# Optimization experiments

Hardware: AMD Instinct MI355X
Metric: run time of the kernel (lower is better)

Reference implementation:

```python
import jax, jax.numpy as jnp
import numpy as np

SIZE = 768
SMALL = SIZE // 4 + 1  # 193
N_ROWS = 16 * 512      # 8192 flattened timesteps
N_CODES = 30000
N_PAIRS = 300000


def setup_inputs() -> dict:
    key = jax.random.key(0)
    ks = jax.random.split(key, 10)
    rnn_output = jax.random.normal(ks[0], (16, 512, SIZE), dtype=jnp.float32)
    weight = jax.random.normal(ks[1], (N_CODES, SIZE + 1), dtype=jnp.float32) * 0.02
    weight1 = jax.random.normal(ks[2], (N_CODES, SMALL), dtype=jnp.float32) * 0.02
    idx0 = jnp.stack([
        jax.random.randint(ks[3], (N_PAIRS,), 0, N_ROWS),
        jax.random.randint(ks[4], (N_PAIRS,), 0, N_CODES),
    ], axis=1).astype(jnp.int64)
    y0 = (jax.random.uniform(ks[5], (N_PAIRS,)) < 0.5).astype(jnp.float32)
    idx1 = jnp.stack([
        jax.random.randint(ks[6], (N_PAIRS,), 0, N_ROWS),
        jax.random.randint(ks[7], (N_PAIRS,), 0, N_CODES),
    ], axis=1).astype(jnp.int64)
    y1 = (jax.random.uniform(ks[8], (N_PAIRS,)) < 0.5).astype(jnp.float32)
    seen0 = jnp.zeros((N_PAIRS,), dtype=jnp.float32)
    seen1 = jnp.zeros((N_PAIRS,), dtype=jnp.float32)
    return {"rnn_output": rnn_output, "weight": weight, "weight1": weight1,
            "idx0": idx0, "y0": y0, "seen0": seen0,
            "idx1": idx1, "y1": y1, "seen1": seen1}


def _embedding_dot(features, table, idx):
    # gather feature rows and code-embedding rows, then row-wise dot -> [N]
    f = features[idx[:, 0]]   # [N, D]
    w = table[idx[:, 1]]      # [N, D]
    return jnp.sum(f * w, axis=-1)


def _bce_logits_sum(logits, targets):
    # stable: log(1 + exp(x)) - x*y, summed
    return jnp.sum(jnp.logaddexp(jnp.float32(0.0), logits) - logits * targets)


def reference(rnn_output, weight, weight1, idx0, y0, seen0, idx1, y1, seen1):
    flat = rnn_output.reshape(-1, SIZE)                     # [B*T, size]
    bias = jnp.ones((flat.shape[0], 1), dtype=flat.dtype)
    rnn_with_bias = jnp.concatenate([flat, bias], axis=1)   # [B*T, size+1]

    final = _embedding_dot(rnn_with_bias, weight, idx0)     # [N]
    loss = _bce_logits_sum(final, y0)

    smaller = rnn_with_bias[:, -SMALL:]                     # [B*T, small]
    final1 = _embedding_dot(smaller, weight1, idx1)         # [N]
    loss1 = _bce_logits_sum(final1, y1)

    return final, loss + loss1
```

## Files before the change

### kernel.cpp

```cpp
#include <hip/hip_runtime.h>
#include <hip/hip_fp16.h>

#define FSIZE   768
#define TW0     769
#define TW1     193
#define COL1    576
#define NPAIRS  300000
#define NCODES  30000
#define NROWS   8192
#define W1STRIDE 200
#define NCB     32768
#define CHUNK   16
#define NWAVES0 (NPAIRS / CHUNK)
#define NB0     ((NWAVES0 + 3) / 4)
#define NWAVES0_PAD (NB0 * 4)
#define NB1     (NPAIRS / 16)
#define NPART   (NWAVES0_PAD + NB1 * 4)

#define SZ_FEAT16 (NROWS * FSIZE / 2)
#define SZ_W116   (NCODES * W1STRIDE / 2)

typedef _Float16 h2_t __attribute__((ext_vector_type(2)));

#if defined(__has_builtin)
# if __has_builtin(__builtin_amdgcn_fdot2)
#  define HAVE_FDOT2 1
# endif
#endif

__device__ __forceinline__ float fdot2f(h2_t a, h2_t b, float c) {
#ifdef HAVE_FDOT2
    return __builtin_amdgcn_fdot2(a, b, c, false);
#else
    return (float)a[0] * (float)b[0] + (float)a[1] * (float)b[1] + c;
#endif
}

__device__ __forceinline__ float loss_term(float x, float y) {
    float ax = fabsf(x);
    return fmaxf(x, 0.0f) + log1pf(__expf(-ax)) - x * y;
}

__device__ __forceinline__ float4 ld4u(const float* p) {
    float4 v; __builtin_memcpy(&v, p, 16); return v;
}

__device__ __forceinline__ void ld2h(const __half* p, h2_t& a, h2_t& b) {
    uint2 u = *(const uint2*)p;
    __builtin_memcpy(&a, &u.x, 4);
    __builtin_memcpy(&b, &u.y, 4);
}

__global__ __launch_bounds__(256) void conv_feat_kernel(
    const float* __restrict__ in, __half* __restrict__ out, int* __restrict__ cnt)
{
    const int gid = blockIdx.x * 256 + threadIdx.x;
    const int i = gid * 4;
    if (i < NROWS * FSIZE) {
        float4 v = *(const float4*)(in + i);
        __half2* o = (__half2*)(out + i);
        o[0] = __floats2half2_rn(v.x, v.y);
        o[1] = __floats2half2_rn(v.z, v.w);
    }
    if (gid < NCB) cnt[gid] = 0;
}

__global__ __launch_bounds__(256) void conv_w1_hist_kernel(
    const float* __restrict__ w1, __half* __restrict__ out,
    const int* __restrict__ idx0, int* __restrict__ cnt)
{
    const int gid = blockIdx.x * 256 + threadIdx.x;
    const int i4 = gid * 4;
    if (i4 < NCODES * W1STRIDE) {
        const int c = i4 / W1STRIDE;
        const int e = i4 - c * W1STRIDE;
        const float* src = w1 + (size_t)c * TW1;
        float v0 = 0.f, v1 = 0.f, v2 = 0.f, v3 = 0.f;
        if (e + 3 < TW1) {
            float4 f = ld4u(src + e);
            v0 = f.x; v1 = f.y; v2 = f.z; v3 = f.w;
        } else {
            if (e     < TW1) v0 = src[e];
            if (e + 1 < TW1) v1 = src[e + 1];
            if (e + 2 < TW1) v2 = src[e + 2];
        }
        __half2* dst = (__half2*)(out + i4);
        dst[0] = __floats2half2_rn(v0, v1);
        dst[1] = __floats2half2_rn(v2, v3);
    }
    if (gid < NPAIRS) atomicAdd(&cnt[idx0[2 * gid + 1]], 1);
}

__global__ __launch_bounds__(256) void hist_kernel(const int* __restrict__ idx,
                                                   int* __restrict__ cnt) {
    int p = blockIdx.x * 256 + threadIdx.x;
    if (p < NPAIRS) atomicAdd(&cnt[idx[2 * p + 1]], 1);
}

__global__ __launch_bounds__(1024) void scan_kernel(const int* __restrict__ cnt,
                                                    int* __restrict__ cursor) {
    __shared__ int sh[1024];
    const int t = threadIdx.x;
    const int4* c4 = (const int4*)cnt + t * 8;
    int4 v[8];
#pragma unroll
    for (int j = 0; j < 8; ++j) v[j] = c4[j];
    int loc[32];
    int s = 0;
#pragma unroll
    for (int j = 0; j < 8; ++j) {
        loc[4 * j + 0] = s; s += v[j].x;
        loc[4 * j + 1] = s; s += v[j].y;
        loc[4 * j + 2] = s; s += v[j].z;
        loc[4 * j + 3] = s; s += v[j].w;
    }
    sh[t] = s;
    __syncthreads();
    for (int off = 1; off < 1024; off <<= 1) {
        int u = (t >= off) ? sh[t - off] : 0;
        __syncthreads();
        sh[t] += u;
        __syncthreads();
    }
    const int base = sh[t] - s;
    int4* cu = (int4*)cursor + t * 8;
#pragma unroll
    for (int j = 0; j < 8; ++j)
        cu[j] = make_int4(base + loc[4 * j], base + loc[4 * j + 1],
                          base + loc[4 * j + 2], base + loc[4 * j + 3]);
}

__global__ __launch_bounds__(256) void scatter_kernel(
    const int* __restrict__ idx, const float* __restrict__ y,
    int* __restrict__ cursor, uint4* __restrict__ srec)
{
    int p = blockIdx.x * 256 + threadIdx.x;
    if (p < NPAIRS) {
        int r = idx[2 * p];
        int c = idx[2 * p + 1];
        int pos = atomicAdd(&cursor[c], 1);
        srec[pos] = make_uint4((unsigned)r, (unsigned)c, __float_as_uint(y[p]), (unsigned)p);
    }
}

template <bool W1H>
__global__ __launch_bounds__(256) void main_kernel(
    const __half* __restrict__ feat16, const float* __restrict__ w0,
    const float* __restrict__ w1f, const __half* __restrict__ w116,
    const uint4* __restrict__ srec,
    const int* __restrict__ idx1, const float* __restrict__ y1,
    float* __restrict__ out_final, float* __restrict__ partial)
{
    const int lane = threadIdx.x & 63;
    const int wv   = threadIdx.x >> 6;

    if (blockIdx.x < NB0) {
        const int wid = blockIdx.x * 4 + wv;
        if (wid >= NWAVES0) { if (lane == 0) partial[wid] = 0.f; return; }
        const uint4 rec = srec[wid * CHUNK + (lane & 15)];

        float lg = 0.f;
        int prev_c = -1;
        h2_t wh0, wh1, wh2, wh3, wh4, wh5;
        float wb = 0.f;

#pragma unroll
        for (int i = 0; i < CHUNK; ++i) {
            const int r = __shfl((int)rec.x, i, 64);
            const int c = __shfl((int)rec.y, i, 64);
            if (c != prev_c) {
                prev_c = c;
                const float* wrow = w0 + (size_t)c * TW0;
                float4 A = ld4u(wrow + 4 * lane);
                float4 B = ld4u(wrow + 4 * lane + 256);
                float4 C = ld4u(wrow + 4 * lane + 512);
                wh0[0] = (_Float16)A.x; wh0[1] = (_Float16)A.y;
                wh1[0] = (_Float16)A.z; wh1[1] = (_Float16)A.w;
                wh2[0] = (_Float16)B.x; wh2[1] = (_Float16)B.y;
                wh3[0] = (_Float16)B.z; wh3[1] = (_Float16)B.w;
                wh4[0] = (_Float16)C.x; wh4[1] = (_Float16)C.y;
                wh5[0] = (_Float16)C.z; wh5[1] = (_Float16)C.w;
                wb = wrow[FSIZE];
            }
            const __half* fr = feat16 + (size_t)r * FSIZE + 4 * lane;
            h2_t a0, a1, a2, a3, a4, a5;
            ld2h(fr, a0, a1);
            ld2h(fr + 256, a2, a3);
            ld2h(fr + 512, a4, a5);
            float s = fdot2f(a0, wh0, 0.f);
            s = fdot2f(a1, wh1, s);
            s = fdot2f(a2, wh2, s);
            s = fdot2f(a3, wh3, s);
            s = fdot2f(a4, wh4, s);
            s = fdot2f(a5, wh5, s);
#pragma unroll
            for (int m = 32; m; m >>= 1) s += __shfl_xor(s, m, 64);
            s += wb;
            lg = (lane == i) ? s : lg;
        }

        float ll = 0.f;
        if (lane < 16) {
            out_final[rec.w] = lg;
            ll = loss_term(lg, __uint_as_float(rec.z));
        }
#pragma unroll
        for (int m = 32; m; m >>= 1) ll += __shfl_xor(ll, m, 64);
        if (lane == 0) partial[wid] = ll;
    } else {
        const int bid  = blockIdx.x - NB0;
        const int sub  = lane & 15;
        const int pair = (bid * 4 + wv) * 4 + (lane >> 4);

        const int r = idx1[2 * pair];
        const int c = idx1[2 * pair + 1];
        const __half* fr = feat16 + (size_t)r * FSIZE + COL1 + 4 * sub;
        h2_t a0, a1, a2, a3, a4, a5;
        ld2h(fr, a0, a1);
        ld2h(fr + 64, a2, a3);
        ld2h(fr + 128, a4, a5);

        float s, bias;
        if (W1H) {
            const __half* wr = w116 + (size_t)c * W1STRIDE;
            h2_t b0, b1, b2, b3, b4, b5;
            ld2h(wr + 4 * sub, b0, b1);
            ld2h(wr + 64 + 4 * sub, b2, b3);
            ld2h(wr + 128 + 4 * sub, b4, b5);
            s = fdot2f(a0, b0, 0.f);
            s = fdot2f(a1, b1, s);
            s = fdot2f(a2, b2, s);
            s = fdot2f(a3, b3, s);
            s = fdot2f(a4, b4, s);
            s = fdot2f(a5, b5, s);
            bias = __half2float(wr[192]);
        } else {
            const float* wr = w1f + (size_t)c * TW1;
            float4 W0 = ld4u(wr + 4 * sub);
            float4 W1 = ld4u(wr + 64 + 4 * sub);
            float4 W2 = ld4u(wr + 128 + 4 * sub);
            s = (float)a0[0] * W0.x + (float)a0[1] * W0.y + (float)a1[0] * W0.z + (float)a1[1] * W0.w
              + (float)a2[0] * W1.x + (float)a2[1] * W1.y + (float)a3[0] * W1.z + (float)a3[1] * W1.w
              + (float)a4[0] * W2.x + (float)a4[1] * W2.y + (float)a5[0] * W2.z + (float)a5[1] * W2.w;
            bias = wr[192];
        }
#pragma unroll
        for (int m = 8; m; m >>= 1) s += __shfl_xor(s, m, 64);
        float ll = (sub == 0) ? loss_term(s + bias, y1[pair]) : 0.f;
#pragma unroll
        for (int m = 32; m; m >>= 1) ll += __shfl_xor(ll, m, 64);
        if (lane == 0) partial[NWAVES0_PAD + bid * 4 + wv] = ll;
    }
}

__global__ __launch_bounds__(1024) void reduce_kernel(
    const float* __restrict__ partial, int n, float* __restrict__ out)
{
    __shared__ float sh[1024];
    float s = 0.0f;
    for (int i = threadIdx.x; i < n; i += 1024) s += partial[i];
    sh[threadIdx.x] = s;
    __syncthreads();
    for (int off = 512; off; off >>= 1) {
        if ((int)threadIdx.x < off) sh[threadIdx.x] += sh[threadIdx.x + off];
        __syncthreads();
    }
    if (threadIdx.x == 0) out[0] = sh[0];
}

__global__ __launch_bounds__(256) void task0_kernel(
    const float* __restrict__ feat, const float* __restrict__ wt,
    const int* __restrict__ idx, const float* __restrict__ y,
    float* __restrict__ out_final, float* __restrict__ partial)
{
    __shared__ float lsum[4];
    const int lane = threadIdx.x & 63;
    const int wv = threadIdx.x >> 6;
    const int pair = blockIdx.x * 4 + wv;
    const int r = idx[2 * pair];
    const int c = idx[2 * pair + 1];
    const float4* f4 = (const float4*)(feat + (size_t)r * FSIZE);
    const float* wrow = wt + (size_t)c * TW0;
    float s = 0.0f;
#pragma unroll
    for (int k = 0; k < 3; ++k) {
        const int j = lane + (k << 6);
        float4 f = f4[j];
        float4 w = ld4u(wrow + 4 * j);
        s += f.x * w.x + f.y * w.y + f.z * w.z + f.w * w.w;
    }
#pragma unroll
    for (int m = 32; m; m >>= 1) s += __shfl_xor(s, m, 64);
    if (lane == 0) {
        const float logit = s + wrow[FSIZE];
        out_final[pair] = logit;
        lsum[wv] = loss_term(logit, y[pair]);
    }
    __syncthreads();
    if (threadIdx.x == 0)
        partial[blockIdx.x] = lsum[0] + lsum[1] + lsum[2] + lsum[3];
}

__global__ __launch_bounds__(256) void task1_kernel(
    const float* __restrict__ feat, const float* __restrict__ wt,
    const int* __restrict__ idx, const float* __restrict__ y,
    float* __restrict__ partial)
{
    __shared__ float lsum[16];
    const int lane = threadIdx.x & 63;
    const int wv = threadIdx.x >> 6;
    const int sub = lane & 15;
    const int pg = lane >> 4;
    const int pair = (blockIdx.x * 4 + wv) * 4 + pg;
    const int r = idx[2 * pair];
    const int c = idx[2 * pair + 1];
    const float4* f4 = (const float4*)(feat + (size_t)r * FSIZE + COL1);
    const float* wrow = wt + (size_t)c * TW1;
    float s = 0.0f;
#pragma unroll
    for (int k = 0; k < 3; ++k) {
        const int j = sub + (k << 4);
        float4 f = f4[j];
        float4 w = ld4u(wrow + 4 * j);
        s += f.x * w.x + f.y * w.y + f.z * w.z + f.w * w.w;
    }
#pragma unroll
    for (int m = 8; m; m >>= 1) s += __shfl_xor(s, m, 64);
    if (sub == 0) {
        const float logit = s + wrow[TW1 - 1];
        lsum[wv * 4 + pg] = loss_term(logit, y[pair]);
    }
    __syncthreads();
    if (threadIdx.x == 0) {
        float t = 0.0f;
#pragma unroll
        for (int i = 0; i < 16; ++i) t += lsum[i];
        partial[blockIdx.x] = t;
    }
}

extern "C" void kernel_launch(void* const* d_in, const int* in_sizes, int n_in,
                              void* d_out, int out_size, void* d_ws, size_t ws_size,
                              hipStream_t stream) {
    const float* feat = (const float*)d_in[0];
    const float* w0   = (const float*)d_in[1];
    const float* w1   = (const float*)d_in[2];
    const int*   idx0 = (const int*)d_in[3];
    const float* y0   = (const float*)d_in[4];
    const int*   idx1 = (const int*)d_in[6];
    const float* y1   = (const float*)d_in[7];

    float* out = (float*)d_out;
    float* ws  = (float*)d_ws;

    const size_t commonU = (size_t)NCB * 2 + (size_t)NPAIRS * 4 + NPART + 64;
    const size_t needA = (SZ_FEAT16 + SZ_W116 + commonU) * 4;
    const size_t needB = (SZ_FEAT16 + commonU) * 4;

    if (ws_size >= needB) {
        const bool tierA = (ws_size >= needA);
        size_t off = 0;
        __half* feat16 = (__half*)(ws + off); off += SZ_FEAT16;
        __half* w116 = nullptr;
        if (tierA) { w116 = (__half*)(ws + off); off += SZ_W116; }
        int* cnt    = (int*)(ws + off); off += NCB;
        int* cursor = (int*)(ws + off); off += NCB;
        uint4* srec = (uint4*)(ws + off); off += (size_t)NPAIRS * 4;
        float* part = ws + off;

        conv_feat_kernel<<<NROWS * FSIZE / 4 / 256, 256, 0, stream>>>(feat, feat16, cnt);
        if (tierA)
            conv_w1_hist_kernel<<<(NCODES * W1STRIDE / 4 + 255) / 256, 256, 0, stream>>>(
                w1, w116, idx0, cnt);
        else
            hist_kernel<<<(NPAIRS + 255) / 256, 256, 0, stream>>>(idx0, cnt);
        scan_kernel<<<1, 1024, 0, stream>>>(cnt, cursor);
        scatter_kernel<<<(NPAIRS + 255) / 256, 256, 0, stream>>>(idx0, y0, cursor, srec);
        if (tierA)
            main_kernel<true><<<NB0 + NB1, 256, 0, stream>>>(
                feat16, w0, w1, w116, srec, idx1, y1, out, part);
        else
            main_kernel<false><<<NB0 + NB1, 256, 0, stream>>>(
                feat16, w0, w1, nullptr, srec, idx1, y1, out, part);
        reduce_kernel<<<1, 1024, 0, stream>>>(part, NPART, out + NPAIRS);
    } else {
        float* part = ws;
        const int nb0 = NPAIRS / 4;
        const int nb1 = NPAIRS / 16;
        task0_kernel<<<nb0, 256, 0, stream>>>(feat, w0, idx0, y0, out, part);
        task1_kernel<<<nb1, 256, 0, stream>>>(feat, w1, idx1, y1, part + nb0);
        reduce_kernel<<<1, 1024, 0, stream>>>(part, nb0 + nb1, out + NPAIRS);
    }
}
```

Before: 187.0 us.

## Split waves into sub-groups per pair, widen loads, shuffle-based scan, per-block partials

The task-0 path now has each 16-lane group handle its own pair (four pairs in flight per wave step), with 16-byte feature loads and fp32 weight rows kept in registers instead of converted to fp16. This shortens the serial 16-step loop and the 64-lane reductions to 4 steps with 16-lane reductions. Task 1 moves from 16 to 8 lanes per pair with 16-byte loads. The scan kernel switches from a shared-memory Hillis-Steele scan to wave shuffles. Loss partials are reduced per block, cutting the partial count. The fp32 weight registers raise register pressure, and the launch-bounds hint targets occupancy.

```diff
diff --git a/kernel.cpp b/kernel.cpp
--- a/kernel.cpp
+++ b/kernel.cpp
@@ -10,12 +10,10 @@
 #define NROWS   8192
 #define W1STRIDE 200
 #define NCB     32768
-#define CHUNK   16
-#define NWAVES0 (NPAIRS / CHUNK)
+#define NWAVES0 (NPAIRS / 16)
 #define NB0     ((NWAVES0 + 3) / 4)
-#define NWAVES0_PAD (NB0 * 4)
-#define NB1     (NPAIRS / 16)
-#define NPART   (NWAVES0_PAD + NB1 * 4)
+#define NB1     (NPAIRS / 32)
+#define NPART   (NB0 + NB1)
 
 #define SZ_FEAT16 (NROWS * FSIZE / 2)
 #define SZ_W116   (NCODES * W1STRIDE / 2)
@@ -45,10 +43,28 @@
     float4 v; __builtin_memcpy(&v, p, 16); return v;
 }
 
-__device__ __forceinline__ void ld2h(const __half* p, h2_t& a, h2_t& b) {
-    uint2 u = *(const uint2*)p;
-    __builtin_memcpy(&a, &u.x, 4);
-    __builtin_memcpy(&b, &u.y, 4);
+__device__ __forceinline__ float acc8(uint4 u, float4 wa, float4 wb, float s) {
+    h2_t h0, h1, h2v, h3;
+    __builtin_memcpy(&h0, &u.x, 4);
+    __builtin_memcpy(&h1, &u.y, 4);
+    __builtin_memcpy(&h2v, &u.z, 4);
+    __builtin_memcpy(&h3, &u.w, 4);
+    s += (float)h0[0] * wa.x; s += (float)h0[1] * wa.y;
+    s += (float)h1[0] * wa.z; s += (float)h1[1] * wa.w;
+    s += (float)h2v[0] * wb.x; s += (float)h2v[1] * wb.y;
+    s += (float)h3[0] * wb.z; s += (float)h3[1] * wb.w;
+    return s;
+}
+
+__device__ __forceinline__ float dot8hh(uint4 a, uint4 b, float s) {
+    h2_t a0, a1, a2, a3, b0, b1, b2, b3;
+    __builtin_memcpy(&a0, &a.x, 4); __builtin_memcpy(&a1, &a.y, 4);
+    __builtin_memcpy(&a2, &a.z, 4); __builtin_memcpy(&a3, &a.w, 4);
+    __builtin_memcpy(&b0, &b.x, 4); __builtin_memcpy(&b1, &b.y, 4);
+    __builtin_memcpy(&b2, &b.z, 4); __builtin_memcpy(&b3, &b.w, 4);
+    s = fdot2f(a0, b0, s); s = fdot2f(a1, b1, s);
+    s = fdot2f(a2, b2, s); s = fdot2f(a3, b3, s);
+    return s;
 }
 
 __global__ __launch_bounds__(256) void conv_feat_kernel(
@@ -99,8 +115,10 @@
 
 __global__ __launch_bounds__(1024) void scan_kernel(const int* __restrict__ cnt,
                                                     int* __restrict__ cursor) {
-    __shared__ int sh[1024];
+    __shared__ int wsum[16];
+    __shared__ int wbase[16];
     const int t = threadIdx.x;
+    const int lane = t & 63, wv = t >> 6;
     const int4* c4 = (const int4*)cnt + t * 8;
     int4 v[8];
 #pragma unroll
@@ -114,15 +132,26 @@
         loc[4 * j + 2] = s; s += v[j].z;
         loc[4 * j + 3] = s; s += v[j].w;
     }
-    sh[t] = s;
-    __syncthreads();
-    for (int off = 1; off < 1024; off <<= 1) {
-        int u = (t >= off) ? sh[t - off] : 0;
-        __syncthreads();
-        sh[t] += u;
-        __syncthreads();
-    }
-    const int base = sh[t] - s;
+    int incl = s;
+#pragma unroll
+    for (int off = 1; off < 64; off <<= 1) {
+        int u = __shfl_up(incl, off, 64);
+        if (lane >= off) incl += u;
+    }
+    if (lane == 63) wsum[wv] = incl;
+    __syncthreads();
+    if (wv == 0 && lane < 16) {
+        int mysum = wsum[lane];
+        int winc = mysum;
+#pragma unroll
+        for (int off = 1; off < 16; off <<= 1) {
+            int u = __shfl_up(winc, off, 64);
+            if (lane >= off) winc += u;
+        }
+        wbase[lane] = winc - mysum;
+    }
+    __syncthreads();
+    const int base = wbase[wv] + incl - s;
     int4* cu = (int4*)cursor + t * 8;
 #pragma unroll
     for (int j = 0; j < 8; ++j)
@@ -144,113 +173,105 @@
 }
 
 template <bool W1H>
-__global__ __launch_bounds__(256) void main_kernel(
+__global__ __launch_bounds__(256, 4) void main_kernel(
     const __half* __restrict__ feat16, const float* __restrict__ w0,
     const float* __restrict__ w1f, const __half* __restrict__ w116,
     const uint4* __restrict__ srec,
     const int* __restrict__ idx1, const float* __restrict__ y1,
     float* __restrict__ out_final, float* __restrict__ partial)
 {
+    __shared__ float bsum[4];
     const int lane = threadIdx.x & 63;
     const int wv   = threadIdx.x >> 6;
+    float wavesum = 0.f;
 
     if (blockIdx.x < NB0) {
         const int wid = blockIdx.x * 4 + wv;
-        if (wid >= NWAVES0) { if (lane == 0) partial[wid] = 0.f; return; }
-        const uint4 rec = srec[wid * CHUNK + (lane & 15)];
-
-        float lg = 0.f;
-        int prev_c = -1;
-        h2_t wh0, wh1, wh2, wh3, wh4, wh5;
-        float wb = 0.f;
-
-#pragma unroll
-        for (int i = 0; i < CHUNK; ++i) {
-            const int r = __shfl((int)rec.x, i, 64);
-            const int c = __shfl((int)rec.y, i, 64);
-            if (c != prev_c) {
-                prev_c = c;
-                const float* wrow = w0 + (size_t)c * TW0;
-                float4 A = ld4u(wrow + 4 * lane);
-                float4 B = ld4u(wrow + 4 * lane + 256);
-                float4 C = ld4u(wrow + 4 * lane + 512);
-                wh0[0] = (_Float16)A.x; wh0[1] = (_Float16)A.y;
-                wh1[0] = (_Float16)A.z; wh1[1] = (_Float16)A.w;
-                wh2[0] = (_Float16)B.x; wh2[1] = (_Float16)B.y;
-                wh3[0] = (_Float16)B.z; wh3[1] = (_Float16)B.w;
-                wh4[0] = (_Float16)C.x; wh4[1] = (_Float16)C.y;
-                wh5[0] = (_Float16)C.z; wh5[1] = (_Float16)C.w;
-                wb = wrow[FSIZE];
+        if (wid < NWAVES0) {
+            const int g = lane >> 4, sub = lane & 15;
+            const uint4 rec = srec[wid * 16 + 4 * g + (sub & 3)];
+            int prev_c = -1;
+            float4 wc[12];
+            float wb = 0.f;
+            float lg = 0.f;
+#pragma unroll
+            for (int j = 0; j < 4; ++j) {
+                const int src = (lane & 48) | j;
+                const int r = __shfl((int)rec.x, src, 64);
+                const int c = __shfl((int)rec.y, src, 64);
+                if (c != prev_c) {
+                    prev_c = c;
+                    const float* wrow = w0 + (size_t)c * TW0 + 8 * sub;
+#pragma unroll
+                    for (int k = 0; k < 6; ++k) {
+                        wc[2 * k]     = ld4u(wrow + 128 * k);
+                        wc[2 * k + 1] = ld4u(wrow + 128 * k + 4);
+                    }
+                    wb = w0[(size_t)c * TW0 + FSIZE];
+                }
+                const __half* fr = feat16 + (size_t)r * FSIZE + 8 * sub;
+                float s = 0.f;
+#pragma unroll
+                for (int k = 0; k < 6; ++k) {
+                    uint4 u = *(const uint4*)(fr + 128 * k);
+                    s = acc8(u, wc[2 * k], wc[2 * k + 1], s);
+                }
+                s += __shfl_xor(s, 8, 64);
+                s += __shfl_xor(s, 4, 64);
+                s += __shfl_xor(s, 2, 64);
+                s += __shfl_xor(s, 1, 64);
+                s += wb;
+                lg = (sub == j) ? s : lg;
             }
-            const __half* fr = feat16 + (size_t)r * FSIZE + 4 * lane;
-            h2_t a0, a1, a2, a3, a4, a5;
-            ld2h(fr, a0, a1);
-            ld2h(fr + 256, a2, a3);
-            ld2h(fr + 512, a4, a5);
-            float s = fdot2f(a0, wh0, 0.f);
-            s = fdot2f(a1, wh1, s);
-            s = fdot2f(a2, wh2, s);
-            s = fdot2f(a3, wh3, s);
-            s = fdot2f(a4, wh4, s);
-            s = fdot2f(a5, wh5, s);
-#pragma unroll
-            for (int m = 32; m; m >>= 1) s += __shfl_xor(s, m, 64);
-            s += wb;
-            lg = (lane == i) ? s : lg;
+            float ll = 0.f;
+            if (sub < 4) {
+                out_final[rec.w] = lg;
+                ll = loss_term(lg, __uint_as_float(rec.z));
+            }
+#pragma unroll
+            for (int m = 32; m; m >>= 1) ll += __shfl_xor(ll, m, 64);
+            wavesum = ll;
         }
-
-        float ll = 0.f;
-        if (lane < 16) {
-            out_final[rec.w] = lg;
-            ll = loss_term(lg, __uint_as_float(rec.z));
-        }
-#pragma unroll
-        for (int m = 32; m; m >>= 1) ll += __shfl_xor(ll, m, 64);
-        if (lane == 0) partial[wid] = ll;
     } else {
         const int bid  = blockIdx.x - NB0;
-        const int sub  = lane & 15;
-        const int pair = (bid * 4 + wv) * 4 + (lane >> 4);
-
+        const int sub  = lane & 7;
+        const int pair = (bid * 4 + wv) * 8 + (lane >> 3);
         const int r = idx1[2 * pair];
         const int c = idx1[2 * pair + 1];
-        const __half* fr = feat16 + (size_t)r * FSIZE + COL1 + 4 * sub;
-        h2_t a0, a1, a2, a3, a4, a5;
-        ld2h(fr, a0, a1);
-        ld2h(fr + 64, a2, a3);
-        ld2h(fr + 128, a4, a5);
-
-        float s, bias;
+        const __half* fr = feat16 + (size_t)r * FSIZE + COL1 + 8 * sub;
+        float s = 0.f;
+        float bias;
         if (W1H) {
-            const __half* wr = w116 + (size_t)c * W1STRIDE;
-            h2_t b0, b1, b2, b3, b4, b5;
-            ld2h(wr + 4 * sub, b0, b1);
-            ld2h(wr + 64 + 4 * sub, b2, b3);
-            ld2h(wr + 128 + 4 * sub, b4, b5);
-            s = fdot2f(a0, b0, 0.f);
-            s = fdot2f(a1, b1, s);
-            s = fdot2f(a2, b2, s);
-            s = fdot2f(a3, b3, s);
-            s = fdot2f(a4, b4, s);
-            s = fdot2f(a5, b5, s);
-            bias = __half2float(wr[192]);
+            const __half* wr = w116 + (size_t)c * W1STRIDE + 8 * sub;
+#pragma unroll
+            for (int k = 0; k < 3; ++k) {
+                uint4 uf = *(const uint4*)(fr + 64 * k);
+                uint4 uw = *(const uint4*)(wr + 64 * k);
+                s = dot8hh(uf, uw, s);
+            }
+            bias = __half2float(w116[(size_t)c * W1STRIDE + 192]);
         } else {
-            const float* wr = w1f + (size_t)c * TW1;
-            float4 W0 = ld4u(wr + 4 * sub);
-            float4 W1 = ld4u(wr + 64 + 4 * sub);
-            float4 W2 = ld4u(wr + 128 + 4 * sub);
-            s = (float)a0[0] * W0.x + (float)a0[1] * W0.y + (float)a1[0] * W0.z + (float)a1[1] * W0.w
-              + (float)a2[0] * W1.x + (float)a2[1] * W1.y + (float)a3[0] * W1.z + (float)a3[1] * W1.w
-              + (float)a4[0] * W2.x + (float)a4[1] * W2.y + (float)a5[0] * W2.z + (float)a5[1] * W2.w;
-            bias = wr[192];
+            const float* wr = w1f + (size_t)c * TW1 + 8 * sub;
+#pragma unroll
+            for (int k = 0; k < 3; ++k) {
+                uint4 uf = *(const uint4*)(fr + 64 * k);
+                s = acc8(uf, ld4u(wr + 64 * k), ld4u(wr + 64 * k + 4), s);
+            }
+            bias = w1f[(size_t)c * TW1 + 192];
         }
-#pragma unroll
-        for (int m = 8; m; m >>= 1) s += __shfl_xor(s, m, 64);
+        s += __shfl_xor(s, 4, 64);
+        s += __shfl_xor(s, 2, 64);
+        s += __shfl_xor(s, 1, 64);
         float ll = (sub == 0) ? loss_term(s + bias, y1[pair]) : 0.f;
 #pragma unroll
         for (int m = 32; m; m >>= 1) ll += __shfl_xor(ll, m, 64);
-        if (lane == 0) partial[NWAVES0_PAD + bid * 4 + wv] = ll;
-    }
+        wavesum = ll;
+    }
+
+    if (lane == 0) bsum[wv] = wavesum;
+    __syncthreads();
+    if (threadIdx.x == 0)
+        partial[blockIdx.x] = bsum[0] + bsum[1] + bsum[2] + bsum[3];
 }
 
 __global__ __launch_bounds__(1024) void reduce_kernel(
```

After: 160.3 us. 14.3% less time.
